# Performance work log

Measured on AMD Instinct MI355X. Metric: run time of the kernel, lower is better.

The kernel has to match this reference:

```python
import jax, jax.numpy as jnp
import numpy as np

B, C, H, W = 4, 256, 64, 64
CQK = C // 2


def setup_inputs() -> dict:
    key = jax.random.key(0)
    ks = jax.random.split(key, 8)
    s = 0.05
    return {
        "x": jax.random.normal(ks[0], (B, C, H, W), dtype=jnp.float32),
        "wq": jax.random.normal(ks[1], (CQK, C), dtype=jnp.float32) * s,
        "bq": jax.random.normal(ks[2], (CQK,), dtype=jnp.float32) * s,
        "wk": jax.random.normal(ks[3], (CQK, C), dtype=jnp.float32) * s,
        "bk": jax.random.normal(ks[4], (CQK,), dtype=jnp.float32) * s,
        "wv": jax.random.normal(ks[5], (C, C), dtype=jnp.float32) * s,
        "bv": jax.random.normal(ks[6], (C,), dtype=jnp.float32) * s,
        "gamma": jax.random.normal(ks[7], (1,), dtype=jnp.float32),
    }


def reference(x, wq, bq, wk, bk, wv, bv, gamma):
    b, c, h, w = x.shape
    n = h * w
    xf = x.reshape(b, c, n)  # [B,C,N]
    # 1x1 convs == per-pixel linear projections
    q = jnp.einsum("oc,bcn->bon", wq, xf) + bq[:, None]  # [B,C/2,N]
    k = jnp.einsum("oc,bcn->bon", wk, xf) + bk[:, None]  # [B,C/2,N]
    v = jnp.einsum("oc,bcn->bon", wv, xf) + bv[:, None]  # [B,C,N]
    # attention[b,m,n'] = softmax_n'( sum_d q[b,d,m] * k[b,d,n'] )
    scores = jnp.einsum("bdm,bdn->bmn", q, k)  # [B,N,N]
    attn = jax.nn.softmax(scores, axis=2)
    # out_feat[b,c,j] = sum_i v[b,c,i] * attn[b,i,j]  (matmul(value, attention))
    af = jnp.einsum("bci,bij->bcj", v, attn)  # [B,C,N]
    out = gamma[0] * af.reshape(b, c, h, w) + x
    return out
```

## Files before the change

### kernel.cpp

```cpp
#include <hip/hip_runtime.h>
#include <hip/hip_bf16.h>


typedef _Float16 f16;
typedef _Float16 f16x4v __attribute__((ext_vector_type(4)));
typedef _Float16 f16x8v __attribute__((ext_vector_type(8)));
typedef float f32x4v __attribute__((ext_vector_type(4)));
typedef unsigned short u16;
typedef unsigned short u16x4v __attribute__((ext_vector_type(4)));
typedef unsigned short u16x8v __attribute__((ext_vector_type(8)));
typedef short s16x8v __attribute__((ext_vector_type(8)));

static __device__ __forceinline__ f32x4v mfma16(f16x8v a, f16x8v b, f32x4v c) {
  return __builtin_amdgcn_mfma_f32_16x16x32_f16(a, b, c, 0, 0, 0);
}
static __device__ __forceinline__ f32x4v mfma_bf(s16x8v a, s16x8v b, f32x4v c) {
  return __builtin_amdgcn_mfma_f32_16x16x32_bf16(a, b, c, 0, 0, 0);
}
static __device__ __forceinline__ u16 f2bf(float f) {
  union { __hip_bfloat16 h; u16 u; } cv;
  cv.h = __float2bfloat16(f);
  return cv.u;
}

#define AS1q __attribute__((address_space(1)))
#define AS3q __attribute__((address_space(3)))
static __device__ __forceinline__ void gl_lds16(const void* g, void* l) {
  __builtin_amdgcn_global_load_lds((const AS1q unsigned int*)g,
                                   (AS3q unsigned int*)l, 16, 0, 0);
}

__global__ void k_wcvt(const float* __restrict__ wq, const float* __restrict__ bq,
                       const float* __restrict__ wk, const float* __restrict__ bk,
                       const float* __restrict__ wv, const float* __restrict__ bv,
                       f16* __restrict__ wh, float* __restrict__ bcat) {
  int o = blockIdx.x;
  int c = threadIdx.x;
  const float* wrow; float bias;
  if (o < 128)      { wrow = wq + (size_t)o * 256;         bias = bq[o]; }
  else if (o < 256) { wrow = wk + (size_t)(o - 128) * 256; bias = bk[o - 128]; }
  else              { wrow = wv + (size_t)(o - 256) * 256; bias = bv[o - 256]; }
  wh[(size_t)o * 256 + c] = (f16)wrow[c];
  if (c == 0) bcat[o] = bias;
}

__global__ void k_xsplit(const float* __restrict__ x, f16* __restrict__ xh) {
  __shared__ float t[64][65];
  int b = blockIdx.z, c0 = blockIdx.y * 64, n0 = blockIdx.x * 64;
  int tx = threadIdx.x & 63, ty = threadIdx.x >> 6;
  const float* xb = x + ((size_t)b * 256 + c0) * 4096 + n0;
#pragma unroll
  for (int r = ty; r < 64; r += 4) t[r][tx] = xb[(size_t)r * 4096 + tx];
  __syncthreads();
  f16* dh = xh + ((size_t)b * 4096 + n0) * 256 + c0;
#pragma unroll
  for (int r = ty; r < 64; r += 4)
    dh[(size_t)r * 256 + tx] = (f16)t[tx][r];
}

__global__ void __launch_bounds__(256, 2)
k_proj(const f16* __restrict__ xh, const f16* __restrict__ wh,
       const float* __restrict__ bcat, f16* __restrict__ qk, f16* __restrict__ vv) {
  extern __shared__ char smem[];
  int b = blockIdx.z, m0 = blockIdx.y * 64, n0 = blockIdx.x * 64;
  int tid = threadIdx.x, l = tid & 63, w = tid >> 6;
  int col = l & 15, quad = l >> 4;
  const f16* Ag = xh + ((size_t)b * 4096 + m0) * 256;
  const f16* Wg = wh + (size_t)n0 * 256;
  int rloc = l >> 5;
  int l5 = l & 31;
#pragma unroll
  for (int p = 0; p < 8; p++) {
    int ci = w * 8 + p;
    int r = ci * 2 + rloc;
    int g = l5 ^ (r & 31);
    gl_lds16(Ag + (size_t)r * 256 + g * 8, smem + ci * 1024);
    gl_lds16(Wg + (size_t)r * 256 + g * 8, smem + 32768 + ci * 1024);
  }
  __syncthreads();
  const char* sA = smem;
  const char* sW = smem + 32768;
  f32x4v acc[4] = {};
  int ar = w * 16 + col;
#pragma unroll
  for (int ks = 0; ks < 8; ks++) {
    int G = ks * 4 + quad;
    f16x8v a = *(const f16x8v*)(sA + ar * 512 + ((G ^ (ar & 31)) * 16));
#pragma unroll
    for (int nt = 0; nt < 4; nt++) {
      int wr = nt * 16 + col;
      f16x8v bb = *(const f16x8v*)(sW + wr * 512 + ((G ^ (wr & 31)) * 16));
      acc[nt] = mfma16(a, bb, acc[nt]);
    }
  }
  bool isqk = (n0 < 256);
#pragma unroll
  for (int nt = 0; nt < 4; nt++) {
    int o = n0 + nt * 16 + col;
    float bias = bcat[o];
    if (isqk) {
#pragma unroll
      for (int rg = 0; rg < 4; rg++) {
        int i = m0 + w * 16 + quad * 4 + rg;
        qk[((size_t)b * 4096 + i) * 256 + o] = (f16)(acc[nt][rg] + bias);
      }
    } else {
      int i = m0 + w * 16 + quad * 4;
      f16x4v pv;
#pragma unroll
      for (int rg = 0; rg < 4; rg++) pv[rg] = (f16)(acc[nt][rg] + bias);
      *(f16x4v*)&vv[((size_t)b * 256 + (o - 256)) * 4096 + i] = pv;
    }
  }
}

__global__ void __launch_bounds__(256, 3)
k_pmake(const f16* __restrict__ qk, u16* __restrict__ P, float* __restrict__ partial) {
  __shared__ char smem[49152];
  f16* sQ = (f16*)smem;
  f16* sK = (f16*)(smem + 32768);
  u16* sPT = (u16*)smem;
  int b = blockIdx.z, i0 = blockIdx.y * 128, j0 = blockIdx.x * 64;
  int tid = threadIdx.x, l = tid & 63, w = tid >> 6;
  int col = l & 15, q = l >> 4;
  const f16* qb = qk + (size_t)b * 4096 * 256;
#pragma unroll
  for (int p = 0; p < 8; p++) {
    int ci = w * 8 + p;
    int r = ci * 4 + (l >> 4);
    int cb = (l & 15) ^ (r & 15);
    gl_lds16(qb + (size_t)(i0 + r) * 256 + cb * 8, smem + ci * 1024);
  }
#pragma unroll
  for (int p = 0; p < 4; p++) {
    int ci = w * 4 + p;
    int r = ci * 4 + (l >> 4);
    int cb = (l & 15) ^ (r & 15);
    gl_lds16(qb + (size_t)(j0 + r) * 256 + 128 + cb * 8, smem + 32768 + ci * 1024);
  }
  __syncthreads();
  f32x4v acc[2][4] = {};
#pragma unroll
  for (int ks = 0; ks < 4; ks++) {
    int phys = (ks * 4 + q) ^ col;
    f16x8v a[2], bb[4];
#pragma unroll
    for (int mt = 0; mt < 2; mt++)
      a[mt] = *(const f16x8v*)&sQ[(w * 32 + mt * 16 + col) * 128 + phys * 8];
#pragma unroll
    for (int nt = 0; nt < 4; nt++)
      bb[nt] = *(const f16x8v*)&sK[(nt * 16 + col) * 128 + phys * 8];
#pragma unroll
    for (int mt = 0; mt < 2; mt++)
#pragma unroll
      for (int nt = 0; nt < 4; nt++)
        acc[mt][nt] = mfma16(a[mt], bb[nt], acc[mt][nt]);
  }
  float pe[2][4][4];
#pragma unroll
  for (int mt = 0; mt < 2; mt++)
#pragma unroll
    for (int nt = 0; nt < 4; nt++)
#pragma unroll
      for (int rg = 0; rg < 4; rg++)
        pe[mt][nt][rg] = __expf(acc[mt][nt][rg]);
  __syncthreads();
#pragma unroll
  for (int mt = 0; mt < 2; mt++) {
    int ib = w * 32 + mt * 16 + q * 4;
#pragma unroll
    for (int nt = 0; nt < 4; nt++) {
      u16x4v pw;
#pragma unroll
      for (int rg = 0; rg < 4; rg++) pw[rg] = f2bf(pe[mt][nt][rg]);
      *(u16x4v*)&sPT[(nt * 16 + col) * 132 + ib] = pw;
    }
  }
#pragma unroll
  for (int mt = 0; mt < 2; mt++) {
    f32x4v cs;
#pragma unroll
    for (int rg = 0; rg < 4; rg++) {
      float t = pe[mt][0][rg] + pe[mt][1][rg] + pe[mt][2][rg] + pe[mt][3][rg];
#pragma unroll
      for (int d = 1; d < 16; d <<= 1) t += __shfl_xor(t, d, 64);
      cs[rg] = t;
    }
    if (col == 0) {
      size_t base = ((size_t)b * 64 + blockIdx.x) * 4096 + i0 + w * 32 + mt * 16 + q * 4;
      *(f32x4v*)&partial[base] = cs;
    }
  }
  __syncthreads();
  u16* Pb = P + ((size_t)b * 4096 + j0) * 4096 + i0;
#pragma unroll
  for (int p = 0; p < 4; p++) {
    int slot = p * 256 + tid;
    int jr = slot >> 4, c16 = slot & 15;
    *(u16x8v*)&Pb[(size_t)jr * 4096 + c16 * 8] =
        *(const u16x8v*)&sPT[jr * 132 + c16 * 8];
  }
}

__global__ void k_rsum(const float* __restrict__ partial, float* __restrict__ rowsum) {
  int b = blockIdx.y;
  int i = blockIdx.x * 256 + threadIdx.x;
  const float* p = partial + (size_t)b * 64 * 4096 + i;
  float s = 0.f;
#pragma unroll 8
  for (int jb = 0; jb < 64; jb++) s += p[(size_t)jb * 4096];
  rowsum[(size_t)b * 4096 + i] = s;
}

__global__ void k_scalev(u16* __restrict__ vvb, const float* __restrict__ rowsum) {
  size_t idx = ((size_t)blockIdx.x * 256 + threadIdx.x) * 8;
  int i = (int)(idx & 4095);
  int b = (int)(idx >> 20);
  f16x8v v = *(f16x8v*)&vvb[idx];
  const float* rs = rowsum + ((size_t)b << 12) + i;
  u16x8v o;
#pragma unroll
  for (int t = 0; t < 8; t++) o[t] = f2bf((float)v[t] * (1.0f / rs[t]));
  *(u16x8v*)&vvb[idx] = o;
}

__global__ void __launch_bounds__(512, 2)
k_av(const u16* __restrict__ vv, const u16* __restrict__ P,
     const float* __restrict__ x, const float* __restrict__ gamma,
     float* __restrict__ out) {
  extern __shared__ char smem[];
  int b = blockIdx.z, c0 = blockIdx.x * 128, j0 = blockIdx.y * 128;
  int tid = threadIdx.x, l = tid & 63, w = tid >> 6;
  int col = l & 15, q = l >> 4;
  int cw = w >> 2, jw = w & 3;
  const u16* Ab = vv + ((size_t)b * 256 + c0) * 4096;
  const u16* Bb = P + ((size_t)b * 4096 + j0) * 4096;
  int rloc = l >> 3;
  int gsw = l & 7;
  f32x4v acc[4][2] = {};
#pragma unroll
  for (int p = 0; p < 4; p++) {
    int ci = w * 4 + p;
    int rr = (ci & 15) * 8 + rloc;
    int g = gsw ^ (rr & 7);
    const u16* src = (ci < 16 ? Ab : Bb) + (size_t)rr * 4096 + g * 8;
    gl_lds16(src, smem + ci * 1024);
  }
  for (int it = 0; it < 64; it++) {
    __syncthreads();
    if (it < 63) {
      int k0 = (it + 1) * 64;
      char* nb = smem + ((it + 1) & 1) * 32768;
#pragma unroll
      for (int p = 0; p < 4; p++) {
        int ci = w * 4 + p;
        int rr = (ci & 15) * 8 + rloc;
        int g = gsw ^ (rr & 7);
        const u16* src = (ci < 16 ? Ab : Bb) + (size_t)rr * 4096 + k0 + g * 8;
        gl_lds16(src, nb + ci * 1024);
      }
    }
    const char* cur = smem + (it & 1) * 32768;
#pragma unroll
    for (int ks = 0; ks < 2; ks++) {
      int G = ks * 4 + q;
      s16x8v a[4], bb[2];
#pragma unroll
      for (int mt = 0; mt < 4; mt++) {
        int ar = cw * 64 + mt * 16 + col;
        a[mt] = *(const s16x8v*)(cur + ar * 128 + ((G ^ (ar & 7)) * 16));
      }
#pragma unroll
      for (int nt = 0; nt < 2; nt++) {
        int jr = jw * 32 + nt * 16 + col;
        bb[nt] = *(const s16x8v*)(cur + 16384 + jr * 128 + ((G ^ (jr & 7)) * 16));
      }
#pragma unroll
      for (int mt = 0; mt < 4; mt++)
#pragma unroll
        for (int nt = 0; nt < 2; nt++)
          acc[mt][nt] = mfma_bf(a[mt], bb[nt], acc[mt][nt]);
    }
  }
  float g = gamma[0];
#pragma unroll
  for (int mt = 0; mt < 4; mt++)
#pragma unroll
    for (int nt = 0; nt < 2; nt++) {
      int c = c0 + cw * 64 + mt * 16 + q * 4;
      int j = j0 + jw * 32 + nt * 16 + col;
#pragma unroll
      for (int rg = 0; rg < 4; rg++) {
        size_t off = ((size_t)b * 256 + c + rg) * 4096 + j;
        out[off] = g * acc[mt][nt][rg] + x[off];
      }
    }
}

extern "C" void kernel_launch(void* const* d_in, const int* in_sizes, int n_in,
                              void* d_out, int out_size, void* d_ws, size_t ws_size,
                              hipStream_t stream) {
  (void)in_sizes; (void)n_in; (void)out_size; (void)ws_size;
  const float* x  = (const float*)d_in[0];
  const float* wq = (const float*)d_in[1];
  const float* bq = (const float*)d_in[2];
  const float* wk = (const float*)d_in[3];
  const float* bk = (const float*)d_in[4];
  const float* wv = (const float*)d_in[5];
  const float* bv = (const float*)d_in[6];
  const float* gm = (const float*)d_in[7];
  float* out = (float*)d_out;

  char* ws = (char*)d_ws;
  const size_t P_BYTES = (size_t)4 * 4096 * 4096 * 2;
  u16*  Pt = (u16*)(ws);
  f16*  xh = (f16*)(ws);
  char* tail = ws + P_BYTES;
  f16*  qk = (f16*)(tail);
  u16*  vv = (u16*)(tail + 8388608);
  f16*  wh = (f16*)(tail + 16777216);
  float* bcat    = (float*)(tail + 17039360);
  float* rowsum  = (float*)(tail + 17041408);
  float* partial = (float*)(tail + 17106944);

  hipLaunchKernelGGL(k_wcvt, dim3(512), dim3(256), 0, stream, wq, bq, wk, bk, wv, bv, wh, bcat);
  hipLaunchKernelGGL(k_xsplit, dim3(64, 4, 4), dim3(256), 0, stream, x, xh);
  hipLaunchKernelGGL(k_proj, dim3(8, 64, 4), dim3(256), 65536, stream, xh, wh, bcat, qk, (f16*)vv);
  hipLaunchKernelGGL(k_pmake, dim3(64, 32, 4), dim3(256), 0, stream, qk, Pt, partial);
  hipLaunchKernelGGL(k_rsum, dim3(16, 4), dim3(256), 0, stream, partial, rowsum);
  hipLaunchKernelGGL(k_scalev, dim3(2048), dim3(256), 0, stream, vv, rowsum);
  hipLaunchKernelGGL(k_av, dim3(2, 32, 4), dim3(512), 65536, stream, vv, Pt, x, gm, out);
}
```

Measured before the change: 204.3 us.

## Fuse score recomputation and exp into AV kernel, drop materialized P matrix

The full 4x4096x4096 bf16 probability matrix is no longer written to and read back from global memory. The first pass now only computes row sums of exp(scores). The AV kernel recomputes Q^T K tiles on the fly, applies exp and the reciprocal row sum, stages the result in LDS as fp16, and multiplies by V. The V scaling kernel is removed. This removes roughly 256 MB of HBM traffic but doubles the QK matmul work, uses 256 single-wave-per-tile workgroups, and moves the AV operands to fp16.

```diff
diff --git a/kernel.cpp b/kernel.cpp
--- a/kernel.cpp
+++ b/kernel.cpp
@@ -6,21 +6,9 @@
 typedef _Float16 f16x4v __attribute__((ext_vector_type(4)));
 typedef _Float16 f16x8v __attribute__((ext_vector_type(8)));
 typedef float f32x4v __attribute__((ext_vector_type(4)));
-typedef unsigned short u16;
-typedef unsigned short u16x4v __attribute__((ext_vector_type(4)));
-typedef unsigned short u16x8v __attribute__((ext_vector_type(8)));
-typedef short s16x8v __attribute__((ext_vector_type(8)));
 
 static __device__ __forceinline__ f32x4v mfma16(f16x8v a, f16x8v b, f32x4v c) {
   return __builtin_amdgcn_mfma_f32_16x16x32_f16(a, b, c, 0, 0, 0);
-}
-static __device__ __forceinline__ f32x4v mfma_bf(s16x8v a, s16x8v b, f32x4v c) {
-  return __builtin_amdgcn_mfma_f32_16x16x32_bf16(a, b, c, 0, 0, 0);
-}
-static __device__ __forceinline__ u16 f2bf(float f) {
-  union { __hip_bfloat16 h; u16 u; } cv;
-  cv.h = __float2bfloat16(f);
-  return cv.u;
 }
 
 #define AS1q __attribute__((address_space(1)))
@@ -115,11 +103,10 @@
 }
 
 __global__ void __launch_bounds__(256, 3)
-k_pmake(const f16* __restrict__ qk, u16* __restrict__ P, float* __restrict__ partial) {
+k_rows(const f16* __restrict__ qk, float* __restrict__ partial) {
   __shared__ char smem[49152];
   f16* sQ = (f16*)smem;
   f16* sK = (f16*)(smem + 32768);
-  u16* sPT = (u16*)smem;
   int b = blockIdx.z, i0 = blockIdx.y * 128, j0 = blockIdx.x * 64;
   int tid = threadIdx.x, l = tid & 63, w = tid >> 6;
   int col = l & 15, q = l >> 4;
@@ -156,32 +143,13 @@
       for (int nt = 0; nt < 4; nt++)
         acc[mt][nt] = mfma16(a[mt], bb[nt], acc[mt][nt]);
   }
-  float pe[2][4][4];
-#pragma unroll
-  for (int mt = 0; mt < 2; mt++)
-#pragma unroll
-    for (int nt = 0; nt < 4; nt++)
-#pragma unroll
-      for (int rg = 0; rg < 4; rg++)
-        pe[mt][nt][rg] = __expf(acc[mt][nt][rg]);
-  __syncthreads();
-#pragma unroll
-  for (int mt = 0; mt < 2; mt++) {
-    int ib = w * 32 + mt * 16 + q * 4;
-#pragma unroll
-    for (int nt = 0; nt < 4; nt++) {
-      u16x4v pw;
-#pragma unroll
-      for (int rg = 0; rg < 4; rg++) pw[rg] = f2bf(pe[mt][nt][rg]);
-      *(u16x4v*)&sPT[(nt * 16 + col) * 132 + ib] = pw;
-    }
-  }
 #pragma unroll
   for (int mt = 0; mt < 2; mt++) {
     f32x4v cs;
 #pragma unroll
     for (int rg = 0; rg < 4; rg++) {
-      float t = pe[mt][0][rg] + pe[mt][1][rg] + pe[mt][2][rg] + pe[mt][3][rg];
+      float t = __expf(acc[mt][0][rg]) + __expf(acc[mt][1][rg]) +
+                __expf(acc[mt][2][rg]) + __expf(acc[mt][3][rg]);
 #pragma unroll
       for (int d = 1; d < 16; d <<= 1) t += __shfl_xor(t, d, 64);
       cs[rg] = t;
@@ -191,108 +159,145 @@
       *(f32x4v*)&partial[base] = cs;
     }
   }
-  __syncthreads();
-  u16* Pb = P + ((size_t)b * 4096 + j0) * 4096 + i0;
-#pragma unroll
-  for (int p = 0; p < 4; p++) {
-    int slot = p * 256 + tid;
-    int jr = slot >> 4, c16 = slot & 15;
-    *(u16x8v*)&Pb[(size_t)jr * 4096 + c16 * 8] =
-        *(const u16x8v*)&sPT[jr * 132 + c16 * 8];
-  }
-}
-
-__global__ void k_rsum(const float* __restrict__ partial, float* __restrict__ rowsum) {
+}
+
+__global__ void k_rsum(const float* __restrict__ partial, float* __restrict__ rinv) {
   int b = blockIdx.y;
   int i = blockIdx.x * 256 + threadIdx.x;
   const float* p = partial + (size_t)b * 64 * 4096 + i;
   float s = 0.f;
 #pragma unroll 8
   for (int jb = 0; jb < 64; jb++) s += p[(size_t)jb * 4096];
-  rowsum[(size_t)b * 4096 + i] = s;
-}
-
-__global__ void k_scalev(u16* __restrict__ vvb, const float* __restrict__ rowsum) {
-  size_t idx = ((size_t)blockIdx.x * 256 + threadIdx.x) * 8;
-  int i = (int)(idx & 4095);
-  int b = (int)(idx >> 20);
-  f16x8v v = *(f16x8v*)&vvb[idx];
-  const float* rs = rowsum + ((size_t)b << 12) + i;
-  u16x8v o;
-#pragma unroll
-  for (int t = 0; t < 8; t++) o[t] = f2bf((float)v[t] * (1.0f / rs[t]));
-  *(u16x8v*)&vvb[idx] = o;
+  rinv[(size_t)b * 4096 + i] = 1.0f / s;
 }
 
 __global__ void __launch_bounds__(512, 2)
-k_av(const u16* __restrict__ vv, const u16* __restrict__ P,
-     const float* __restrict__ x, const float* __restrict__ gamma,
-     float* __restrict__ out) {
+k_fav(const f16* __restrict__ qk, const f16* __restrict__ vv,
+      const float* __restrict__ rinv, const float* __restrict__ x,
+      const float* __restrict__ gamma, float* __restrict__ out) {
   extern __shared__ char smem[];
-  int b = blockIdx.z, c0 = blockIdx.x * 128, j0 = blockIdx.y * 128;
+  f16* sE = (f16*)(smem + 98304);
+  int wg = blockIdx.x;
+  int lg = (wg & 7) * 32 + (wg >> 3);
+  int b = lg >> 6, j0 = (lg & 63) * 64;
   int tid = threadIdx.x, l = tid & 63, w = tid >> 6;
-  int col = l & 15, q = l >> 4;
-  int cw = w >> 2, jw = w & 3;
-  const u16* Ab = vv + ((size_t)b * 256 + c0) * 4096;
-  const u16* Bb = P + ((size_t)b * 4096 + j0) * 4096;
-  int rloc = l >> 3;
-  int gsw = l & 7;
-  f32x4v acc[4][2] = {};
+  int col = l & 15, quad = l >> 4;
+  int ti = w & 3;
+  int tjb = (w >> 2) * 2;
+  const f16* qb = qk + (size_t)b * 4096 * 256;
+  const f16* vb = vv + (size_t)b * 256 * 4096;
+  const float* rp = rinv + (size_t)b * 4096 + ti * 16 + col;
+
+#pragma unroll
+  for (int p = 0; p < 2; p++) {
+    int ci = w * 2 + p;
+    int r = ci * 4 + (l >> 4);
+    int cb = (l & 15) ^ (r & 15);
+    gl_lds16(qb + (size_t)(j0 + r) * 256 + 128 + cb * 8, smem + ci * 1024);
+  }
+  __syncthreads();
+  f16x8v ka[2][4];
+  {
+    const f16* sK0 = (const f16*)smem;
+#pragma unroll
+    for (int t = 0; t < 2; t++)
+#pragma unroll
+      for (int ks = 0; ks < 4; ks++)
+        ka[t][ks] = *(const f16x8v*)&sK0[((tjb + t) * 16 + col) * 128 +
+                                         (((ks * 4 + quad) ^ col) * 8)];
+  }
+  __syncthreads();
+#pragma unroll
+  for (int p = 0; p < 2; p++) {
+    int ci = w * 2 + p;
+    int r = ci * 4 + (l >> 4);
+    int cb = (l & 15) ^ (r & 15);
+    gl_lds16(qb + (size_t)r * 256 + cb * 8, smem + ci * 1024);
+  }
 #pragma unroll
   for (int p = 0; p < 4; p++) {
     int ci = w * 4 + p;
-    int rr = (ci & 15) * 8 + rloc;
-    int g = gsw ^ (rr & 7);
-    const u16* src = (ci < 16 ? Ab : Bb) + (size_t)rr * 4096 + g * 8;
-    gl_lds16(src, smem + ci * 1024);
-  }
+    int rr = ci * 8 + (l >> 3);
+    int g = (l & 7) ^ (rr & 7);
+    gl_lds16(vb + (size_t)rr * 4096 + g * 8, smem + 32768 + ci * 1024);
+  }
+
+  f32x4v acc[2][4] = {};
+  int ig = ti * 2 + (col >> 3);
   for (int it = 0; it < 64; it++) {
+    int cur = it & 1;
     __syncthreads();
     if (it < 63) {
-      int k0 = (it + 1) * 64;
-      char* nb = smem + ((it + 1) & 1) * 32768;
+      int i1 = (it + 1) * 64;
+      char* nq = smem + ((it + 1) & 1) * 16384;
+      char* nv = smem + 32768 + ((it + 1) & 1) * 32768;
+#pragma unroll
+      for (int p = 0; p < 2; p++) {
+        int ci = w * 2 + p;
+        int r = ci * 4 + (l >> 4);
+        int cb = (l & 15) ^ (r & 15);
+        gl_lds16(qb + (size_t)(i1 + r) * 256 + cb * 8, nq + ci * 1024);
+      }
 #pragma unroll
       for (int p = 0; p < 4; p++) {
         int ci = w * 4 + p;
-        int rr = (ci & 15) * 8 + rloc;
-        int g = gsw ^ (rr & 7);
-        const u16* src = (ci < 16 ? Ab : Bb) + (size_t)rr * 4096 + k0 + g * 8;
-        gl_lds16(src, nb + ci * 1024);
-      }
-    }
-    const char* cur = smem + (it & 1) * 32768;
+        int rr = ci * 8 + (l >> 3);
+        int g = (l & 7) ^ (rr & 7);
+        gl_lds16(vb + (size_t)rr * 4096 + i1 + g * 8, nv + ci * 1024);
+      }
+    }
+    const f16* sQc = (const f16*)(smem + cur * 16384);
+    const f16* sVc = (const f16*)(smem + 32768 + cur * 32768);
+    f32x4v accs[2] = {};
+#pragma unroll
+    for (int ks = 0; ks < 4; ks++) {
+      f16x8v qf = *(const f16x8v*)&sQc[(ti * 16 + col) * 128 +
+                                       (((ks * 4 + quad) ^ col) * 8)];
+      accs[0] = mfma16(ka[0][ks], qf, accs[0]);
+      accs[1] = mfma16(ka[1][ks], qf, accs[1]);
+    }
+    float rv = rp[it * 64];
+#pragma unroll
+    for (int t = 0; t < 2; t++)
+#pragma unroll
+      for (int rg = 0; rg < 4; rg++) {
+        float e = __expf(accs[t][rg]) * rv;
+        int jl = (tjb + t) * 16 + quad * 4 + rg;
+        sE[jl * 64 + ((ig ^ (jl & 7)) * 8) + (col & 7)] = (f16)e;
+      }
+    asm volatile("s_waitcnt lgkmcnt(0)\n\ts_barrier" ::: "memory");
 #pragma unroll
     for (int ks = 0; ks < 2; ks++) {
-      int G = ks * 4 + q;
-      s16x8v a[4], bb[2];
-#pragma unroll
-      for (int mt = 0; mt < 4; mt++) {
-        int ar = cw * 64 + mt * 16 + col;
-        a[mt] = *(const s16x8v*)(cur + ar * 128 + ((G ^ (ar & 7)) * 16));
-      }
-#pragma unroll
-      for (int nt = 0; nt < 2; nt++) {
-        int jr = jw * 32 + nt * 16 + col;
-        bb[nt] = *(const s16x8v*)(cur + 16384 + jr * 128 + ((G ^ (jr & 7)) * 16));
-      }
-#pragma unroll
-      for (int mt = 0; mt < 4; mt++)
-#pragma unroll
-        for (int nt = 0; nt < 2; nt++)
-          acc[mt][nt] = mfma_bf(a[mt], bb[nt], acc[mt][nt]);
-    }
-  }
-  float g = gamma[0];
-#pragma unroll
-  for (int mt = 0; mt < 4; mt++)
-#pragma unroll
-    for (int nt = 0; nt < 2; nt++) {
-      int c = c0 + cw * 64 + mt * 16 + q * 4;
-      int j = j0 + jw * 32 + nt * 16 + col;
+      int sw = ((ks * 4 + quad) ^ (col & 7)) * 8;
+      f16x8v va0 = *(const f16x8v*)&sVc[(w * 32 + col) * 64 + sw];
+      f16x8v va1 = *(const f16x8v*)&sVc[(w * 32 + 16 + col) * 64 + sw];
+      f16x8v e0 = *(const f16x8v*)&sE[col * 64 + sw];
+      f16x8v e1 = *(const f16x8v*)&sE[(16 + col) * 64 + sw];
+      f16x8v e2 = *(const f16x8v*)&sE[(32 + col) * 64 + sw];
+      f16x8v e3 = *(const f16x8v*)&sE[(48 + col) * 64 + sw];
+      acc[0][0] = mfma16(va0, e0, acc[0][0]);
+      acc[0][1] = mfma16(va0, e1, acc[0][1]);
+      acc[0][2] = mfma16(va0, e2, acc[0][2]);
+      acc[0][3] = mfma16(va0, e3, acc[0][3]);
+      acc[1][0] = mfma16(va1, e0, acc[1][0]);
+      acc[1][1] = mfma16(va1, e1, acc[1][1]);
+      acc[1][2] = mfma16(va1, e2, acc[1][2]);
+      acc[1][3] = mfma16(va1, e3, acc[1][3]);
+    }
+  }
+  float gm = gamma[0];
+  const float* xb = x + (size_t)b * 256 * 4096;
+  float* ob = out + (size_t)b * 256 * 4096;
+#pragma unroll
+  for (int mt = 0; mt < 2; mt++)
+#pragma unroll
+    for (int jt = 0; jt < 4; jt++) {
+      int c = w * 32 + mt * 16 + quad * 4;
+      int j = j0 + jt * 16 + col;
 #pragma unroll
       for (int rg = 0; rg < 4; rg++) {
-        size_t off = ((size_t)b * 256 + c + rg) * 4096 + j;
-        out[off] = g * acc[mt][nt][rg] + x[off];
+        size_t off = (size_t)(c + rg) * 4096 + j;
+        ob[off] = gm * acc[mt][jt][rg] + xb[off];
       }
     }
 }
@@ -312,22 +317,18 @@
   float* out = (float*)d_out;
 
   char* ws = (char*)d_ws;
-  const size_t P_BYTES = (size_t)4 * 4096 * 4096 * 2;
-  u16*  Pt = (u16*)(ws);
-  f16*  xh = (f16*)(ws);
-  char* tail = ws + P_BYTES;
-  f16*  qk = (f16*)(tail);
-  u16*  vv = (u16*)(tail + 8388608);
-  f16*  wh = (f16*)(tail + 16777216);
-  float* bcat    = (float*)(tail + 17039360);
-  float* rowsum  = (float*)(tail + 17041408);
-  float* partial = (float*)(tail + 17106944);
+  f16*  xh = (f16*)ws;
+  f16*  qk = (f16*)(ws + 8388608);
+  f16*  vv = (f16*)(ws + 16777216);
+  f16*  wh = (f16*)(ws + 25165824);
+  float* bcat    = (float*)(ws + 25427968);
+  float* rinv    = (float*)(ws + 25430016);
+  float* partial = (float*)(ws + 25495552);
 
   hipLaunchKernelGGL(k_wcvt, dim3(512), dim3(256), 0, stream, wq, bq, wk, bk, wv, bv, wh, bcat);
   hipLaunchKernelGGL(k_xsplit, dim3(64, 4, 4), dim3(256), 0, stream, x, xh);
-  hipLaunchKernelGGL(k_proj, dim3(8, 64, 4), dim3(256), 65536, stream, xh, wh, bcat, qk, (f16*)vv);
-  hipLaunchKernelGGL(k_pmake, dim3(64, 32, 4), dim3(256), 0, stream, qk, Pt, partial);
-  hipLaunchKernelGGL(k_rsum, dim3(16, 4), dim3(256), 0, stream, partial, rowsum);
-  hipLaunchKernelGGL(k_scalev, dim3(2048), dim3(256), 0, stream, vv, rowsum);
-  hipLaunchKernelGGL(k_av, dim3(2, 32, 4), dim3(512), 65536, stream, vv, Pt, x, gm, out);
-}
+  hipLaunchKernelGGL(k_proj, dim3(8, 64, 4), dim3(256), 65536, stream, xh, wh, bcat, qk, vv);
+  hipLaunchKernelGGL(k_rows, dim3(64, 32, 4), dim3(256), 0, stream, qk, partial);
+  hipLaunchKernelGGL(k_rsum, dim3(16, 4), dim3(256), 0, stream, partial, rinv);
+  hipLaunchKernelGGL(k_fav, dim3(256), dim3(512), 106496, stream, qk, vv, rinv, x, gm, out);
+}
```

After: 225.5 us. 10.4% more time.
